# Kernel optimization log

Hardware: AMD Instinct MI355X
Metric: run time of the kernel (lower is better)

Reference implementation:

```python
import jax, jax.numpy as jnp
import numpy as np

N_NODES = 100000
N_EDGES = 500000
E_DIM = 128  # embedding_channels
OUT_DIM = 1


def setup_inputs() -> dict:
    key = jax.random.key(0)
    k_z, k_ei, k_w1, k_w2 = jax.random.split(key, 4)
    z = jax.random.normal(k_z, (N_NODES, E_DIM), dtype=jnp.float32)
    edge_label_index = jax.random.randint(k_ei, (2, N_EDGES), 0, N_NODES, dtype=jnp.int64)
    # MLP([2E, E, out]) params, kaiming-ish scale
    W1 = jax.random.normal(k_w1, (2 * E_DIM, E_DIM), dtype=jnp.float32) * (2.0 / (2 * E_DIM)) ** 0.5
    b1 = jnp.zeros((E_DIM,), dtype=jnp.float32)
    W2 = jax.random.normal(k_w2, (E_DIM, OUT_DIM), dtype=jnp.float32) * (2.0 / E_DIM) ** 0.5
    b2 = jnpp = jnp.zeros((OUT_DIM,), dtype=jnp.float32)
    return {"z": z, "edge_label_index": edge_label_index,
            "W1": W1, "b1": b1, "W2": W2, "b2": b2}


def reference(z, edge_label_index, W1, b1, W2, b2):
    # gather endpoint embeddings and concat: [n_edges, 2E]
    src = z[edge_label_index[0]]  # [n_edges, E]
    dst = z[edge_label_index[1]]  # [n_edges, E]
    x = jnp.concatenate([src, dst], axis=-1)
    # MLP: Linear(2E->E) -> ReLU -> Linear(E->out)
    h = jax.nn.relu(x @ W1 + b1)
    return h @ W2 + b2
```

## Files before the change

kernel.cpp:

```cpp
#include <hip/hip_runtime.h>
#include <hip/hip_bf16.h>

#define N_NODES 100000
#define N_EDGES 500000
#define EDIM 128

using bf16x8 = __attribute__((ext_vector_type(8))) __bf16;
using f32x4  = __attribute__((ext_vector_type(4))) float;

__global__ void cvt_z_kernel(const float* __restrict__ z, __bf16* __restrict__ zb) {
    int i = blockIdx.x * blockDim.x + threadIdx.x;
    const float4* p = (const float4*)z + (size_t)i * 2;
    float4 a = p[0], b = p[1];
    bf16x8 o;
    o[0] = (__bf16)a.x; o[1] = (__bf16)a.y; o[2] = (__bf16)a.z; o[3] = (__bf16)a.w;
    o[4] = (__bf16)b.x; o[5] = (__bf16)b.y; o[6] = (__bf16)b.z; o[7] = (__bf16)b.w;
    ((bf16x8*)zb)[i] = o;
}

__global__ void cvt_w1_kernel(const float* __restrict__ W1, __bf16* __restrict__ w1f) {
    int t = blockIdx.x * blockDim.x + threadIdx.x;
    int lane = t & 63, frag = t >> 6;
    int kt = frag >> 3, nt = frag & 7;
    int k0 = kt * 32 + (lane >> 4) * 8;
    int n  = nt * 16 + (lane & 15);
    bf16x8 o;
#pragma unroll
    for (int i = 0; i < 8; i++) o[i] = (__bf16)W1[(k0 + i) * 128 + n];
    ((bf16x8*)w1f)[t] = o;
}

__global__ __launch_bounds__(256, 2) void decode_kernel(
    const __bf16* __restrict__ zb, const __bf16* __restrict__ w1f,
    const int* __restrict__ ei, const float* __restrict__ b1,
    const float* __restrict__ W2, const float* __restrict__ b2,
    float* __restrict__ out)
{
    __shared__ __bf16 sW[64 * 512];
    {
        const uint4* src = (const uint4*)w1f;
        uint4* dst = (uint4*)sW;
#pragma unroll
        for (int i = 0; i < 16; i++)
            dst[threadIdx.x + 256 * i] = src[threadIdx.x + 256 * i];
    }
    __syncthreads();

    const int lane = threadIdx.x & 63;
    const int wave = threadIdx.x >> 6;
    const int l15 = lane & 15, l4 = lane >> 4;
    const long long ebase = (long long)blockIdx.x * 256 + wave * 64;

    const __bf16* aptr[4][2];
#pragma unroll
    for (int mt = 0; mt < 4; mt++) {
        long long e = ebase + mt * 16 + l15;
        if (e >= N_EDGES) e = N_EDGES - 1;
        int si = ei[e];
        int di = ei[N_EDGES + e];
        aptr[mt][0] = zb + (size_t)si * EDIM + l4 * 8;
        aptr[mt][1] = zb + (size_t)di * EDIM + l4 * 8;
    }

    const f32x4 zero = {0.f, 0.f, 0.f, 0.f};
    f32x4 acc[4][8];
#pragma unroll
    for (int mt = 0; mt < 4; mt++)
#pragma unroll
        for (int nt = 0; nt < 8; nt++) acc[mt][nt] = zero;

#pragma unroll
    for (int kt = 0; kt < 8; kt++) {
        bf16x8 bfr[8];
#pragma unroll
        for (int nt = 0; nt < 8; nt++)
            bfr[nt] = *(const bf16x8*)&sW[(kt * 8 + nt) * 512 + lane * 8];
        const int half = kt >> 2;
        const int ko   = (kt & 3) * 32;
#pragma unroll
        for (int mt = 0; mt < 4; mt++) {
            bf16x8 a = *(const bf16x8*)(aptr[mt][half] + ko);
#pragma unroll
            for (int nt = 0; nt < 8; nt++)
                acc[mt][nt] = __builtin_amdgcn_mfma_f32_16x16x32_bf16(a, bfr[nt], acc[mt][nt], 0, 0, 0);
        }
    }

    float b1v[8], w2v[8];
#pragma unroll
    for (int nt = 0; nt < 8; nt++) {
        int c = nt * 16 + l15;
        b1v[nt] = b1[c];
        w2v[nt] = W2[c];
    }
    const float bias2 = b2[0];

#pragma unroll
    for (int mt = 0; mt < 4; mt++) {
#pragma unroll
        for (int j = 0; j < 4; j++) {
            float p = 0.f;
#pragma unroll
            for (int nt = 0; nt < 8; nt++)
                p += fmaxf(acc[mt][nt][j] + b1v[nt], 0.f) * w2v[nt];
            p += __shfl_xor(p, 1, 64);
            p += __shfl_xor(p, 2, 64);
            p += __shfl_xor(p, 4, 64);
            p += __shfl_xor(p, 8, 64);
            long long e = ebase + mt * 16 + l4 * 4 + j;
            if (l15 == 0 && e < N_EDGES) out[e] = p + bias2;
        }
    }
}

extern "C" void kernel_launch(void* const* d_in, const int* in_sizes, int n_in,
                              void* d_out, int out_size, void* d_ws, size_t ws_size,
                              hipStream_t stream) {
    const float* z  = (const float*)d_in[0];
    const int*   ei = (const int*)d_in[1];
    const float* W1 = (const float*)d_in[2];
    const float* b1 = (const float*)d_in[3];
    const float* W2 = (const float*)d_in[4];
    const float* b2 = (const float*)d_in[5];
    float* out = (float*)d_out;

    __bf16* zb  = (__bf16*)d_ws;
    __bf16* w1f = (__bf16*)((char*)d_ws + (size_t)N_NODES * EDIM * 2);

    cvt_z_kernel<<<(N_NODES * EDIM / 8) / 256, 256, 0, stream>>>(z, zb);
    cvt_w1_kernel<<<16, 256, 0, stream>>>(W1, w1f);
    decode_kernel<<<(N_EDGES + 255) / 256, 256, 0, stream>>>(zb, w1f, ei, b1, W2, b2, out);
}
```

Baseline: 152.9 us.

## Precompute per-node projections of W1 halves, then gather and sum per edge

Splits the first linear layer algebraically: each node's embedding is multiplied once by both halves of W1, producing a [N_NODES, 256] bf16 table, instead of running a 256-wide GEMM per edge. The edge kernel then gathers the source half and destination half, adds the bias, applies ReLU and takes the dot with W2. GEMM work drops from 500k edges to 100k nodes, and the separate z-to-bf16 conversion pass is folded into the node GEMM. In exchange the intermediate table (about 51 MB) has to be written and then randomly gathered, and rounding the pre-activation sums to bf16 adds some extra error.

After: 154.4 us. No clear change (+0.9%).

```diff
diff --git a/kernel.cpp b/kernel.cpp
--- a/kernel.cpp
+++ b/kernel.cpp
@@ -3,38 +3,30 @@
 
 #define N_NODES 100000
 #define N_EDGES 500000
-#define EDIM 128
 
 using bf16x8 = __attribute__((ext_vector_type(8))) __bf16;
 using f32x4  = __attribute__((ext_vector_type(4))) float;
 
-__global__ void cvt_z_kernel(const float* __restrict__ z, __bf16* __restrict__ zb) {
-    int i = blockIdx.x * blockDim.x + threadIdx.x;
-    const float4* p = (const float4*)z + (size_t)i * 2;
-    float4 a = p[0], b = p[1];
-    bf16x8 o;
-    o[0] = (__bf16)a.x; o[1] = (__bf16)a.y; o[2] = (__bf16)a.z; o[3] = (__bf16)a.w;
-    o[4] = (__bf16)b.x; o[5] = (__bf16)b.y; o[6] = (__bf16)b.z; o[7] = (__bf16)b.w;
-    ((bf16x8*)zb)[i] = o;
-}
 
-__global__ void cvt_w1_kernel(const float* __restrict__ W1, __bf16* __restrict__ w1f) {
-    int t = blockIdx.x * blockDim.x + threadIdx.x;
+__global__ void cvt_w1f_kernel(const float* __restrict__ W1, __bf16* __restrict__ w1f) {
+    int t = blockIdx.x * 256 + threadIdx.x;
     int lane = t & 63, frag = t >> 6;
-    int kt = frag >> 3, nt = frag & 7;
-    int k0 = kt * 32 + (lane >> 4) * 8;
+    int kq = frag >> 4, nt = frag & 15;
+    int k0 = kq * 32 + (lane >> 4) * 8;
     int n  = nt * 16 + (lane & 15);
     bf16x8 o;
 #pragma unroll
-    for (int i = 0; i < 8; i++) o[i] = (__bf16)W1[(k0 + i) * 128 + n];
+    for (int i = 0; i < 8; i++) {
+        int k = k0 + i;
+        float w = (n < 128) ? W1[k * 128 + n] : W1[(k + 128) * 128 + (n - 128)];
+        o[i] = (__bf16)w;
+    }
     ((bf16x8*)w1f)[t] = o;
 }
 
-__global__ __launch_bounds__(256, 2) void decode_kernel(
-    const __bf16* __restrict__ zb, const __bf16* __restrict__ w1f,
-    const int* __restrict__ ei, const float* __restrict__ b1,
-    const float* __restrict__ W2, const float* __restrict__ b2,
-    float* __restrict__ out)
+__global__ __launch_bounds__(256, 2) void node_gemm_kernel(
+    const float* __restrict__ z, const __bf16* __restrict__ w1f,
+    __bf16* __restrict__ C)
 {
     __shared__ __bf16 sW[64 * 512];
     {
@@ -49,17 +41,15 @@
     const int lane = threadIdx.x & 63;
     const int wave = threadIdx.x >> 6;
     const int l15 = lane & 15, l4 = lane >> 4;
-    const long long ebase = (long long)blockIdx.x * 256 + wave * 64;
+    const int wr = wave >> 1, wc = wave & 1;
+    const int rowbase = blockIdx.x * 128 + wr * 64;
 
-    const __bf16* aptr[4][2];
+    const float* arow[4];
 #pragma unroll
     for (int mt = 0; mt < 4; mt++) {
-        long long e = ebase + mt * 16 + l15;
-        if (e >= N_EDGES) e = N_EDGES - 1;
-        int si = ei[e];
-        int di = ei[N_EDGES + e];
-        aptr[mt][0] = zb + (size_t)si * EDIM + l4 * 8;
-        aptr[mt][1] = zb + (size_t)di * EDIM + l4 * 8;
+        int r = rowbase + mt * 16 + l15;
+        if (r >= N_NODES) r = N_NODES - 1;
+        arow[mt] = z + (size_t)r * 128 + l4 * 8;
     }
 
     const f32x4 zero = {0.f, 0.f, 0.f, 0.f};
@@ -70,45 +60,84 @@
         for (int nt = 0; nt < 8; nt++) acc[mt][nt] = zero;
 
 #pragma unroll
-    for (int kt = 0; kt < 8; kt++) {
+    for (int kq = 0; kq < 4; kq++) {
         bf16x8 bfr[8];
 #pragma unroll
-        for (int nt = 0; nt < 8; nt++)
-            bfr[nt] = *(const bf16x8*)&sW[(kt * 8 + nt) * 512 + lane * 8];
-        const int half = kt >> 2;
-        const int ko   = (kt & 3) * 32;
+        for (int nt = 0; nt < 8; nt++) {
+            int fid = kq * 16 + wc * 8 + nt;
+            bfr[nt] = *(const bf16x8*)&sW[fid * 512 + lane * 8];
+        }
 #pragma unroll
         for (int mt = 0; mt < 4; mt++) {
-            bf16x8 a = *(const bf16x8*)(aptr[mt][half] + ko);
+            const float4* p = (const float4*)(arow[mt] + kq * 32);
+            float4 x0 = p[0], x1 = p[1];
+            bf16x8 a;
+            a[0] = (__bf16)x0.x; a[1] = (__bf16)x0.y; a[2] = (__bf16)x0.z; a[3] = (__bf16)x0.w;
+            a[4] = (__bf16)x1.x; a[5] = (__bf16)x1.y; a[6] = (__bf16)x1.z; a[7] = (__bf16)x1.w;
 #pragma unroll
             for (int nt = 0; nt < 8; nt++)
                 acc[mt][nt] = __builtin_amdgcn_mfma_f32_16x16x32_bf16(a, bfr[nt], acc[mt][nt], 0, 0, 0);
         }
     }
 
-    float b1v[8], w2v[8];
-#pragma unroll
-    for (int nt = 0; nt < 8; nt++) {
-        int c = nt * 16 + l15;
-        b1v[nt] = b1[c];
-        w2v[nt] = W2[c];
-    }
-    const float bias2 = b2[0];
-
 #pragma unroll
     for (int mt = 0; mt < 4; mt++) {
 #pragma unroll
         for (int j = 0; j < 4; j++) {
+            int r = rowbase + mt * 16 + l4 * 4 + j;
+            if (r < N_NODES) {
+#pragma unroll
+                for (int nt = 0; nt < 8; nt++)
+                    C[(size_t)r * 256 + wc * 128 + nt * 16 + l15] = (__bf16)acc[mt][nt][j];
+            }
+        }
+    }
+}
+
+__global__ __launch_bounds__(256, 4) void edge_kernel(
+    const __bf16* __restrict__ C, const int* __restrict__ ei,
+    const float* __restrict__ b1, const float* __restrict__ W2,
+    const float* __restrict__ b2, float* __restrict__ out)
+{
+    const int lane = threadIdx.x & 63;
+    const int wave = threadIdx.x >> 6;
+    const int g = lane >> 4, sub = lane & 15;
+
+    const float4* b1p = (const float4*)(b1 + sub * 8);
+    const float4* w2p = (const float4*)(W2 + sub * 8);
+    float4 bb0 = b1p[0], bb1 = b1p[1];
+    float4 ww0 = w2p[0], ww1 = w2p[1];
+    float b1v[8] = {bb0.x, bb0.y, bb0.z, bb0.w, bb1.x, bb1.y, bb1.z, bb1.w};
+    float w2v[8] = {ww0.x, ww0.y, ww0.z, ww0.w, ww1.x, ww1.y, ww1.z, ww1.w};
+    const float bias2 = b2[0];
+
+    const int wid = blockIdx.x * 4 + wave;
+    const int nw  = gridDim.x * 4;
+
+    for (long long eb = (long long)wid * 16; eb < N_EDGES; eb += (long long)nw * 16) {
+        bf16x8 cu[4], cv[4];
+        long long e[4];
+#pragma unroll
+        for (int q = 0; q < 4; q++) {
+            e[q] = eb + q * 4 + g;
+            int is = ei[e[q]];
+            int id = ei[N_EDGES + e[q]];
+            cu[q] = *(const bf16x8*)(C + (size_t)is * 256 + sub * 8);
+            cv[q] = *(const bf16x8*)(C + (size_t)id * 256 + 128 + sub * 8);
+        }
+#pragma unroll
+        for (int q = 0; q < 4; q++) {
             float p = 0.f;
 #pragma unroll
-            for (int nt = 0; nt < 8; nt++)
-                p += fmaxf(acc[mt][nt][j] + b1v[nt], 0.f) * w2v[nt];
+            for (int i = 0; i < 8; i++) {
+                float h = (float)cu[q][i] + (float)cv[q][i] + b1v[i];
+                p += fmaxf(h, 0.f) * w2v[i];
+            }
             p += __shfl_xor(p, 1, 64);
             p += __shfl_xor(p, 2, 64);
             p += __shfl_xor(p, 4, 64);
             p += __shfl_xor(p, 8, 64);
-            long long e = ebase + mt * 16 + l4 * 4 + j;
-            if (l15 == 0 && e < N_EDGES) out[e] = p + bias2;
+            if (sub == 0) out[e[q]] = p + bias2;
         }
     }
 }
@@ -124,10 +153,10 @@
     const float* b2 = (const float*)d_in[5];
     float* out = (float*)d_out;
 
-    __bf16* zb  = (__bf16*)d_ws;
-    __bf16* w1f = (__bf16*)((char*)d_ws + (size_t)N_NODES * EDIM * 2);
+    __bf16* w1f = (__bf16*)d_ws;
+    __bf16* Cbuf = (__bf16*)((char*)d_ws + 65536);
 
-    cvt_z_kernel<<<(N_NODES * EDIM / 8) / 256, 256, 0, stream>>>(z, zb);
-    cvt_w1_kernel<<<16, 256, 0, stream>>>(W1, w1f);
-    decode_kernel<<<(N_EDGES + 255) / 256, 256, 0, stream>>>(zb, w1f, ei, b1, W2, b2, out);
+    cvt_w1f_kernel<<<16, 256, 0, stream>>>(W1, w1f);
+    node_gemm_kernel<<<(N_NODES + 127) / 128, 256, 0, stream>>>(z, w1f, Cbuf);
+    edge_kernel<<<2048, 256, 0, stream>>>(Cbuf, ei, b1, W2, b2, out);
 }
```
